# Kernel tuning notes

Measured on AMD Instinct MI355X. Metric: run time of the kernel, lower is better.

## Reference

```python
import jax, jax.numpy as jnp
import numpy as np

B, A, M = 16, 65536, 64
TIMELINE = 10000.0


def setup_inputs() -> dict:
    key = jax.random.key(0)
    k1, k2, k3, k4, k5 = jax.random.split(key, 5)
    # anchor intervals [start, end] on a 1D timeline
    a_ctr = jax.random.uniform(k1, (A,)) * TIMELINE
    a_w = 20.0 + jax.random.uniform(k2, (A,)) * 40.0
    anchor = jnp.stack([a_ctr - 0.5 * a_w, a_ctr + 0.5 * a_w], axis=1)  # [A,2]
    anchors = anchor[None]  # [1,A,2]
    # ground-truth annotations [start, end, class]; class 0 => all valid
    g_ctr = jax.random.uniform(k3, (B, M)) * TIMELINE
    g_w = 20.0 + jax.random.uniform(k4, (B, M)) * 40.0
    annotations = jnp.stack(
        [g_ctr - 0.5 * g_w, g_ctr + 0.5 * g_w, jnp.zeros((B, M))], axis=2
    )  # [B,M,3]
    regressions = jax.random.normal(k5, (B, A, 2))  # predicted (dx, dw)
    return {"regressions": regressions, "anchors": anchors, "annotations": annotations}


def reference(regressions, anchors, annotations):
    anchor = anchors[0]                         # [A,2]
    aw = anchor[:, 1] - anchor[:, 0]            # anchor widths
    actr = anchor[:, 0] + 0.5 * aw              # anchor centers
    third = 1.0 / 9.0                           # smooth-L1 transition (sigma^2 = 9)

    def per_image(reg, ann):                    # reg [A,2], ann [M,3]
        valid = ann[:, 2] != -1.0               # [M] class != -1
        boxes = ann[:, :2]                      # [M,2]
        area = boxes[:, 1] - boxes[:, 0]        # [M]
        # pairwise 1D IoU [A,M]
        iw = jnp.minimum(anchor[:, 1:2], boxes[None, :, 1]) - jnp.maximum(
            anchor[:, 0:1], boxes[None, :, 0])
        iw = jnp.clip(iw, 0.0)
        ua = jnp.clip(aw[:, None] + area[None, :] - iw, 1e-8)
        iou = iw / ua
        iou = jnp.where(valid[None, :], iou, -1.0)  # invalid annots never matched
        iou_max = iou.max(axis=1)               # [A]
        iou_arg = iou.argmax(axis=1)            # [A]
        pos = iou_max >= 0.5                    # positive anchors [A]
        assigned = boxes[iou_arg]               # [A,2] assigned GT per anchor
        gw = assigned[:, 1] - assigned[:, 0]
        gctr = assigned[:, 0] + 0.5 * gw
        gw = jnp.clip(gw, 1.0)
        tdx = (gctr - actr) / aw / 0.1          # targets / [0.1, 0.2]
        tdw = jnp.log(gw / aw) / 0.2
        targets = jnp.stack([tdx, tdw], axis=1)  # [A,2]
        diff = jnp.abs(targets - reg)
        sl1 = jnp.where(diff <= third, 0.5 * 9.0 * diff * diff, diff - 0.5 / 9.0)
        npos = pos.sum()
        # mean over positive rows (both columns), 0 if no positives / no valid annots
        loss = (sl1 * pos[:, None].astype(sl1.dtype)).sum() / (
            2.0 * jnp.maximum(npos, 1).astype(sl1.dtype))
        loss = jnp.where(npos > 0, loss, 0.0)
        loss = jnp.where(valid.any(), loss, 0.0)
        return loss

    losses = jax.vmap(per_image)(regressions, annotations)  # [B]
    return losses.mean(keepdims=True)  # [1]
```

## Files before the change

kernel.cpp:

```cpp
#include <hip/hip_runtime.h>

#define B_IMG 16
#define A_N   65536
#define M_N   64
#define BLK   256
#define APT   4
#define BLOCKS_PER_IMG (A_N / (BLK * APT))
#define NSLOT (B_IMG * BLOCKS_PER_IMG)
#define NBINS 160
#define INV_BINW (1.0f / 64.0f)
#define MARGIN 30.5f

__global__ __launch_bounds__(256) void rl_main(
    const float* __restrict__ reg,
    const float2* __restrict__ anchors,
    const float* __restrict__ ann,
    float2* __restrict__ partials,
    int atomic_mode)
{
    __shared__ float4 sboxes[M_N];
    __shared__ int    soff[NBINS + 1];
    __shared__ int    sbin[M_N];
    const int b   = blockIdx.y;
    const int bx  = blockIdx.x;
    const int tid = threadIdx.x;

    float b0 = 0.f, b1 = 0.f;
    if (tid < M_N) {
        const float* p = ann + (b * M_N + tid) * 3;
        b0 = p[0]; b1 = p[1];
        float v = p[2];
        float gctr = b0 + 0.5f * (b1 - b0);
        int bin = (int)floorf(gctr * INV_BINW);
        bin = min(max(bin, 0), NBINS - 1);
        sbin[tid] = (v != -1.0f) ? bin : NBINS;
    }
    __syncthreads();

    if (tid < M_N) {
        const int mybin = sbin[tid];
        int rank = 0;
        #pragma unroll 8
        for (int m = 0; m < M_N; ++m) {
            int bm = sbin[m];
            rank += (bm < mybin) || (bm == mybin && m < tid);
        }
        sboxes[rank] = make_float4(b0, b1, b1 - b0, 0.0f);
    }
    if (tid <= NBINS) {
        int cnt = 0;
        #pragma unroll 8
        for (int m = 0; m < M_N; ++m)
            cnt += (sbin[m] < tid);
        soff[tid] = cnt;
    }
    __syncthreads();

    const int abase = bx * (BLK * APT) + tid;
    float lsum = 0.0f, lcnt = 0.0f;

    #pragma unroll
    for (int j = 0; j < APT; ++j) {
        const float2 an = anchors[abase + j * BLK];
        const float ax = an.x, ay = an.y, aw = ay - ax;
        int lo = (int)floorf((ax - MARGIN) * INV_BINW);
        int hi = (int)floorf((ay + MARGIN) * INV_BINW);
        lo = max(lo, 0);
        hi = min(hi, NBINS - 1);
        int k    = soff[lo];
        const int kend = soff[hi + 1];

        float biw = 0.0f, bua = 1.0f;
        int   bidx = 0;
        for (; k < kend; ++k) {
            const float4 g = sboxes[k];
            float iw = fminf(ay, g.y) - fmaxf(ax, g.x);
            iw = fmaxf(iw, 0.0f);
            float ua = (aw + g.z) - iw;
            if (iw * bua > biw * ua) { biw = iw; bua = ua; bidx = k; }
        }

        if (biw >= 0.5f * bua) {
            lcnt += 1.0f;
            const float4 g = sboxes[bidx];
            float gw   = g.y - g.x;
            float gctr = g.x + 0.5f * gw;
            gw = fmaxf(gw, 1.0f);
            float actr = ax + 0.5f * aw;
            float tdx = (gctr - actr) / aw / 0.1f;
            float tdw = logf(gw / aw) / 0.2f;
            const float2 r = ((const float2*)reg)[(size_t)b * A_N + abase + j * BLK];
            float d0 = fabsf(tdx - r.x);
            float d1 = fabsf(tdw - r.y);
            const float third = 1.0f / 9.0f;
            lsum += (d0 <= third) ? 4.5f * d0 * d0 : d0 - (0.5f / 9.0f);
            lsum += (d1 <= third) ? 4.5f * d1 * d1 : d1 - (0.5f / 9.0f);
        }
    }

    #pragma unroll
    for (int off = 32; off > 0; off >>= 1) {
        lsum += __shfl_down(lsum, off, 64);
        lcnt += __shfl_down(lcnt, off, 64);
    }
    __shared__ float rs[4], rc[4];
    const int wave = tid >> 6, lane = tid & 63;
    if (lane == 0) { rs[wave] = lsum; rc[wave] = lcnt; }
    __syncthreads();
    if (tid == 0) {
        float s = rs[0] + rs[1] + rs[2] + rs[3];
        float c = rc[0] + rc[1] + rc[2] + rc[3];
        if (atomic_mode) {
            atomicAdd(&((float*)partials)[b * 2 + 0], s);
            atomicAdd(&((float*)partials)[b * 2 + 1], c);
        } else {
            partials[b * BLOCKS_PER_IMG + bx] = make_float2(s, c);
        }
    }
}

__global__ __launch_bounds__(1024) void rl_final_p(
    const float2* __restrict__ partials, float* __restrict__ out)
{
    __shared__ float simg[B_IMG];
    const int tid = threadIdx.x;
    const int w = tid >> 6, l = tid & 63;
    float2 p = partials[w * BLOCKS_PER_IMG + l];
    float s = p.x, c = p.y;
    #pragma unroll
    for (int off = 32; off > 0; off >>= 1) {
        s += __shfl_down(s, off, 64);
        c += __shfl_down(c, off, 64);
    }
    if (l == 0)
        simg[w] = (c > 0.0f) ? s / (2.0f * fmaxf(c, 1.0f)) : 0.0f;
    __syncthreads();
    if (tid == 0) {
        float t = 0.0f;
        #pragma unroll
        for (int i = 0; i < B_IMG; ++i) t += simg[i];
        out[0] = t * (1.0f / (float)B_IMG);
    }
}

__global__ void rl_final_a(const float* __restrict__ ws, float* __restrict__ out)
{
    const int tid = threadIdx.x;
    float loss = 0.0f;
    if (tid < B_IMG) {
        float s = ws[tid * 2 + 0], c = ws[tid * 2 + 1];
        loss = (c > 0.0f) ? s / (2.0f * fmaxf(c, 1.0f)) : 0.0f;
    }
    #pragma unroll
    for (int off = 32; off > 0; off >>= 1)
        loss += __shfl_down(loss, off, 64);
    if (tid == 0) out[0] = loss * (1.0f / (float)B_IMG);
}

extern "C" void kernel_launch(void* const* d_in, const int* in_sizes, int n_in,
                              void* d_out, int out_size, void* d_ws, size_t ws_size,
                              hipStream_t stream)
{
    const float*  reg     = (const float*)d_in[0];
    const float2* anchors = (const float2*)d_in[1];
    const float*  ann     = (const float*)d_in[2];
    float* out = (float*)d_out;

    const size_t need = NSLOT * sizeof(float2);
    dim3 grid(BLOCKS_PER_IMG, B_IMG);

    if (ws_size >= need) {
        float2* partials = (float2*)d_ws;
        rl_main<<<grid, dim3(BLK), 0, stream>>>(reg, anchors, ann, partials, 0);
        rl_final_p<<<1, dim3(B_IMG * 64), 0, stream>>>(partials, out);
    } else {
        hipMemsetAsync(d_ws, 0, 2 * B_IMG * sizeof(float), stream);
        rl_main<<<grid, dim3(BLK), 0, stream>>>(reg, anchors, ann, (float2*)d_ws, 1);
        rl_final_a<<<1, 64, 0, stream>>>((const float*)d_ws, out);
    }
}
```

Before: 69.33 us.

## Fuse final reduction into main kernel via last-block atomic counter

Replaces the per-block partials buffer and separate finalize kernel with per-image atomic accumulators. A global completion counter lets the last block compute the mean loss, so one kernel launch is removed (a memset is added). It also doubles anchors per thread, which halves the block count, and runs the bin-offset prefix computation in parallel with the box ranking on separate threads. The trade-offs are atomic contention, a memset every call, fewer blocks to fill the GPU, and float atomics whose summation order is nondeterministic.

```diff
diff --git a/kernel.cpp b/kernel.cpp
--- a/kernel.cpp
+++ b/kernel.cpp
@@ -4,23 +4,25 @@
 #define A_N   65536
 #define M_N   64
 #define BLK   256
-#define APT   4
+#define APT   8
 #define BLOCKS_PER_IMG (A_N / (BLK * APT))
-#define NSLOT (B_IMG * BLOCKS_PER_IMG)
+#define NBLOCKS (B_IMG * BLOCKS_PER_IMG)
 #define NBINS 160
 #define INV_BINW (1.0f / 64.0f)
 #define MARGIN 30.5f
 
-__global__ __launch_bounds__(256) void rl_main(
+__global__ __launch_bounds__(256) void rl_fused(
     const float* __restrict__ reg,
     const float2* __restrict__ anchors,
     const float* __restrict__ ann,
-    float2* __restrict__ partials,
-    int atomic_mode)
+    float* __restrict__ img_acc,
+    int* __restrict__ counter,
+    float* __restrict__ out)
 {
     __shared__ float4 sboxes[M_N];
     __shared__ int    soff[NBINS + 1];
     __shared__ int    sbin[M_N];
+    __shared__ int    sdone;
     const int b   = blockIdx.y;
     const int bx  = blockIdx.x;
     const int tid = threadIdx.x;
@@ -46,13 +48,13 @@
             rank += (bm < mybin) || (bm == mybin && m < tid);
         }
         sboxes[rank] = make_float4(b0, b1, b1 - b0, 0.0f);
-    }
-    if (tid <= NBINS) {
+    } else if (tid < 64 + NBINS + 1) {
+        const int t = tid - 64;
         int cnt = 0;
         #pragma unroll 8
         for (int m = 0; m < M_N; ++m)
-            cnt += (sbin[m] < tid);
-        soff[tid] = cnt;
+            cnt += (sbin[m] < t);
+        soff[t] = cnt;
     }
     __syncthreads();
 
@@ -63,10 +65,8 @@
     for (int j = 0; j < APT; ++j) {
         const float2 an = anchors[abase + j * BLK];
         const float ax = an.x, ay = an.y, aw = ay - ax;
-        int lo = (int)floorf((ax - MARGIN) * INV_BINW);
-        int hi = (int)floorf((ay + MARGIN) * INV_BINW);
-        lo = max(lo, 0);
-        hi = min(hi, NBINS - 1);
+        int lo = max((int)((ax - MARGIN) * INV_BINW), 0);
+        int hi = min((int)((ay + MARGIN) * INV_BINW), NBINS - 1);
         int k    = soff[lo];
         const int kend = soff[hi + 1];
 
@@ -110,51 +110,30 @@
     if (tid == 0) {
         float s = rs[0] + rs[1] + rs[2] + rs[3];
         float c = rc[0] + rc[1] + rc[2] + rc[3];
-        if (atomic_mode) {
-            atomicAdd(&((float*)partials)[b * 2 + 0], s);
-            atomicAdd(&((float*)partials)[b * 2 + 1], c);
-        } else {
-            partials[b * BLOCKS_PER_IMG + bx] = make_float2(s, c);
+        atomicAdd(&img_acc[b * 2 + 0], s);
+        atomicAdd(&img_acc[b * 2 + 1], c);
+        __threadfence();
+        int old = atomicAdd(counter, 1);
+        sdone = (old == NBLOCKS - 1);
+    }
+    __syncthreads();
+
+    if (sdone) {
+        float loss = 0.0f;
+        if (tid < B_IMG) {
+            float s = __hip_atomic_load(&img_acc[tid * 2 + 0],
+                                        __ATOMIC_ACQUIRE, __HIP_MEMORY_SCOPE_AGENT);
+            float c = __hip_atomic_load(&img_acc[tid * 2 + 1],
+                                        __ATOMIC_ACQUIRE, __HIP_MEMORY_SCOPE_AGENT);
+            loss = (c > 0.0f) ? s / (2.0f * fmaxf(c, 1.0f)) : 0.0f;
+        }
+        if (tid < 64) {
+            #pragma unroll
+            for (int off = 32; off > 0; off >>= 1)
+                loss += __shfl_down(loss, off, 64);
+            if (tid == 0) out[0] = loss * (1.0f / (float)B_IMG);
         }
     }
-}
-
-__global__ __launch_bounds__(1024) void rl_final_p(
-    const float2* __restrict__ partials, float* __restrict__ out)
-{
-    __shared__ float simg[B_IMG];
-    const int tid = threadIdx.x;
-    const int w = tid >> 6, l = tid & 63;
-    float2 p = partials[w * BLOCKS_PER_IMG + l];
-    float s = p.x, c = p.y;
-    #pragma unroll
-    for (int off = 32; off > 0; off >>= 1) {
-        s += __shfl_down(s, off, 64);
-        c += __shfl_down(c, off, 64);
-    }
-    if (l == 0)
-        simg[w] = (c > 0.0f) ? s / (2.0f * fmaxf(c, 1.0f)) : 0.0f;
-    __syncthreads();
-    if (tid == 0) {
-        float t = 0.0f;
-        #pragma unroll
-        for (int i = 0; i < B_IMG; ++i) t += simg[i];
-        out[0] = t * (1.0f / (float)B_IMG);
-    }
-}
-
-__global__ void rl_final_a(const float* __restrict__ ws, float* __restrict__ out)
-{
-    const int tid = threadIdx.x;
-    float loss = 0.0f;
-    if (tid < B_IMG) {
-        float s = ws[tid * 2 + 0], c = ws[tid * 2 + 1];
-        loss = (c > 0.0f) ? s / (2.0f * fmaxf(c, 1.0f)) : 0.0f;
-    }
-    #pragma unroll
-    for (int off = 32; off > 0; off >>= 1)
-        loss += __shfl_down(loss, off, 64);
-    if (tid == 0) out[0] = loss * (1.0f / (float)B_IMG);
 }
 
 extern "C" void kernel_launch(void* const* d_in, const int* in_sizes, int n_in,
@@ -166,16 +145,11 @@
     const float*  ann     = (const float*)d_in[2];
     float* out = (float*)d_out;
 
-    const size_t need = NSLOT * sizeof(float2);
+    float* img_acc = (float*)d_ws;
+    int*   counter = (int*)((char*)d_ws + 128);
+
+    hipMemsetAsync(d_ws, 0, 132, stream);
+
     dim3 grid(BLOCKS_PER_IMG, B_IMG);
-
-    if (ws_size >= need) {
-        float2* partials = (float2*)d_ws;
-        rl_main<<<grid, dim3(BLK), 0, stream>>>(reg, anchors, ann, partials, 0);
-        rl_final_p<<<1, dim3(B_IMG * 64), 0, stream>>>(partials, out);
-    } else {
-        hipMemsetAsync(d_ws, 0, 2 * B_IMG * sizeof(float), stream);
-        rl_main<<<grid, dim3(BLK), 0, stream>>>(reg, anchors, ann, (float2*)d_ws, 1);
-        rl_final_a<<<1, 64, 0, stream>>>((const float*)d_ws, out);
-    }
+    rl_fused<<<grid, dim3(BLK), 0, stream>>>(reg, anchors, ann, img_acc, counter, out);
 }
```

Measured after the change: 83.53 us. 1.2x slower.
